# Kernel optimization log

Hardware: AMD Instinct MI355X
Metric: run time of the kernel (lower is better)

## Reference

```python
import jax, jax.numpy as jnp
import numpy as np

B, T, P, F = 32, 12, 128, 128          # batch, timesteps, n_patches, nhid
NODES_PER_PATCH = 64
HORIZON = 12
N_NODES = P * NODES_PER_PATCH          # 8192


def setup_inputs() -> dict:
    key = jax.random.key(0)
    k1, k2, k3, k4 = jax.random.split(key, 4)
    x = jax.random.normal(k1, (B, T, P, F), dtype=jnp.float32)
    # per-patch Linear weights/biases, stacked: W[p] maps (nhid*T) -> (nodes_p*horizon)
    W = jax.random.normal(k2, (P, T * F, NODES_PER_PATCH * HORIZON), dtype=jnp.float32) * 0.02
    b = jax.random.normal(k3, (P, NODES_PER_PATCH * HORIZON), dtype=jnp.float32) * 0.02
    # patch -> global node indices; a permutation (each node in exactly one patch)
    patch_node_map = jax.random.permutation(k4, jnp.arange(N_NODES, dtype=jnp.int64)).reshape(P, NODES_PER_PATCH)
    return {"x": x, "W": W, "b": b, "patch_node_map": patch_node_map}


def reference(x, W, b, patch_node_map):
    # rearrange 'b t p f -> b p (t f)'
    xr = jnp.transpose(x, (0, 2, 1, 3)).reshape(x.shape[0], P, T * F)
    # grouped GEMM: one Linear per patch
    out = jnp.einsum('bpi,pio->bpo', xr, W) + b          # [B, P, nodes*H]
    out = out.reshape(x.shape[0], P * NODES_PER_PATCH, HORIZON)
    # scatter patch-local node predictions to global node positions
    out_all = jnp.zeros((x.shape[0], N_NODES, HORIZON), dtype=x.dtype)
    out_all = out_all.at[:, patch_node_map.reshape(-1), :].set(out)
    return out_all
```

## Files before the change

### kernel.cpp

```cpp
#include <hip/hip_runtime.h>
#include <hip/hip_bf16.h>


constexpr int T      = 12;
constexpr int P      = 128;
constexpr int F      = 128;
constexpr int K      = T * F;
constexpr int N      = 768;
constexpr int NPP    = 64;
constexpr int H      = 12;
constexpr int NNODES = P * NPP;
constexpr int BN     = 384;
constexpr int NSTEP  = 48;
constexpr int TPF    = T * P * F;
constexpr int PF     = P * F;

typedef __attribute__((ext_vector_type(8))) short        bf16x8;
typedef __attribute__((ext_vector_type(4))) float        f32x4;
typedef __attribute__((ext_vector_type(4))) unsigned int u32x4;

__device__ inline unsigned short f2bfu(float f) {
    return __bfloat16_as_ushort(__float2bfloat16(f));
}
__device__ inline unsigned int pk2(float lo, float hi) {
    return (unsigned int)f2bfu(lo) | ((unsigned int)f2bfu(hi) << 16);
}

__global__ __launch_bounds__(384, 1)
void patch_readout_kernel(const float* __restrict__ x,
                          const float* __restrict__ W,
                          const float* __restrict__ bias,
                          const int*   __restrict__ map,
                          float*       __restrict__ out)
{
    __shared__ short Xs[32 * K];
    __shared__ short Ws2[2][4 * BN * 8];
    char* xl  = (char*)&Xs[0];
    char* wlb = (char*)&Ws2[0][0];

    const int bid = blockIdx.x;
    const int lgc = (bid & 7) * 32 + (bid >> 3);
    const int p   = lgc >> 1;
    const int n0  = (lgc & 1) * BN;

    const int tid  = threadIdx.x;
    const int lane = tid & 63;
    const int wv   = tid >> 6;
    const int r    = lane & 15;
    const int c    = lane >> 4;

    const int c2 = tid / 96;
    const int q  = tid - c2 * 96;
    const float* wg = W + (size_t)p * K * N + (size_t)(8 * c2) * N + (n0 + 4 * q);

    f32x4 ws[8];

    auto issueW = [&](int s) {
        #pragma unroll
        for (int j = 0; j < 8; ++j)
            ws[j] = *(const f32x4*)(wg + (size_t)(s * 32 + j) * N);
    };

    auto writeW = [&](int d) {
        char* wl = wlb + d * 24576 + c2 * 6144;
        #pragma unroll
        for (int i = 0; i < 4; ++i) {
            u32x4 wd;
            wd.x = pk2(ws[0][i], ws[1][i]);
            wd.y = pk2(ws[2][i], ws[3][i]);
            wd.z = pk2(ws[4][i], ws[5][i]);
            wd.w = pk2(ws[6][i], ws[7][i]);
            const int col = 4 * q + i;
            *(u32x4*)(wl + ((col * 16) ^ (((col >> 3) & 7) << 4))) = wd;
        }
    };

    auto stageX = [&]() {
        const int row = tid / 12;
        const int sub = tid - row * 12;
        const float* xg = x + (size_t)row * TPF + (size_t)sub * PF + (size_t)p * F;
        char* xw = xl + row * 3072;
        const int sw = (row & 7) << 4;
        #pragma unroll
        for (int ci = 0; ci < 16; ++ci) {
            f32x4 v0 = *(const f32x4*)(xg + ci * 8);
            f32x4 v1 = *(const f32x4*)(xg + ci * 8 + 4);
            bf16x8 xv;
            xv[0] = (short)f2bfu(v0.x); xv[1] = (short)f2bfu(v0.y);
            xv[2] = (short)f2bfu(v0.z); xv[3] = (short)f2bfu(v0.w);
            xv[4] = (short)f2bfu(v1.x); xv[5] = (short)f2bfu(v1.y);
            xv[6] = (short)f2bfu(v1.z); xv[7] = (short)f2bfu(v1.w);
            *(bf16x8*)(xw + ((sub * 256 + ci * 16) ^ sw)) = xv;
        }
    };

    f32x4 acc[2][4] = {};

    auto compute = [&](int s, int d) {
        const char* wl = wlb + d * 24576 + c * 6144;
        bf16x8 af[2];
        #pragma unroll
        for (int mi = 0; mi < 2; ++mi) {
            const int row = mi * 16 + r;
            af[mi] = *(const bf16x8*)(xl + row * 3072 +
                                      ((s * 64 + c * 16) ^ ((row & 7) << 4)));
        }
        #pragma unroll
        for (int ni = 0; ni < 4; ++ni) {
            const int col = wv * 64 + ni * 16 + r;
            bf16x8 bf = *(const bf16x8*)(wl + ((col * 16) ^ (((col >> 3) & 7) << 4)));
            #pragma unroll
            for (int mi = 0; mi < 2; ++mi)
                acc[mi][ni] = __builtin_amdgcn_mfma_f32_16x16x32_bf16(
                    af[mi], bf, acc[mi][ni], 0, 0, 0);
        }
    };

    issueW(0);
    stageX();
    writeW(0);

    for (int s = 0; s < NSTEP; ++s) {
        __syncthreads();
        if (s < NSTEP - 1) issueW(s + 1);
        compute(s, s & 1);
        if (s < NSTEP - 1) writeW((s + 1) & 1);
    }

    #pragma unroll
    for (int ni = 0; ni < 4; ++ni) {
        const int col = n0 + wv * 64 + ni * 16 + r;
        const int nl  = col / H;
        const int h   = col - nl * H;
        const int g   = map[p * NPP + nl];
        const float bv = bias[p * N + col];
        #pragma unroll
        for (int mi = 0; mi < 2; ++mi) {
            #pragma unroll
            for (int i = 0; i < 4; ++i) {
                const int b = mi * 16 + c * 4 + i;
                out[((size_t)b * NNODES + g) * H + h] = acc[mi][ni][i] + bv;
            }
        }
    }
}

extern "C" void kernel_launch(void* const* d_in, const int* in_sizes, int n_in,
                              void* d_out, int out_size, void* d_ws, size_t ws_size,
                              hipStream_t stream) {
    const float* x    = (const float*)d_in[0];
    const float* W    = (const float*)d_in[1];
    const float* bias = (const float*)d_in[2];
    const int*   map  = (const int*)d_in[3];
    float*       out  = (float*)d_out;

    dim3 grid(256);
    dim3 block(384);
    patch_readout_kernel<<<grid, block, 0, stream>>>(x, W, bias, map, out);
}
```

Baseline: 125.2 us.

## Split-K grouped GEMM into two halves with bf16 workspace reduction kernel

```diff
diff --git a/kernel.cpp b/kernel.cpp
--- a/kernel.cpp
+++ b/kernel.cpp
@@ -10,10 +10,12 @@
 constexpr int NPP    = 64;
 constexpr int H      = 12;
 constexpr int NNODES = P * NPP;
-constexpr int BN     = 384;
-constexpr int NSTEP  = 48;
+constexpr int KH2    = 768;
+constexpr int NSTEP2 = KH2 / 32;
 constexpr int TPF    = T * P * F;
 constexpr int PF     = P * F;
+constexpr size_t HALF_ELE = (size_t)P * 32 * N;
+constexpr size_t WS_BYTES = 2 * HALF_ELE * 2;
 
 typedef __attribute__((ext_vector_type(8))) short        bf16x8;
 typedef __attribute__((ext_vector_type(4))) float        f32x4;
@@ -25,23 +27,23 @@
 __device__ inline unsigned int pk2(float lo, float hi) {
     return (unsigned int)f2bfu(lo) | ((unsigned int)f2bfu(hi) << 16);
 }
+__device__ inline f32x4 ntload(const float* p) {
+    return __builtin_nontemporal_load((const f32x4*)p);
+}
 
 __global__ __launch_bounds__(384, 1)
-void patch_readout_kernel(const float* __restrict__ x,
-                          const float* __restrict__ W,
-                          const float* __restrict__ bias,
-                          const int*   __restrict__ map,
-                          float*       __restrict__ out)
+void pr_phase1(const float* __restrict__ x, const float* __restrict__ W,
+               __hip_bfloat16* __restrict__ wsp_out)
 {
-    __shared__ short Xs[32 * K];
-    __shared__ short Ws2[2][4 * BN * 8];
+    __shared__ short Xs[32 * KH2];
+    __shared__ short Ws2[2][4 * N * 8];
     char* xl  = (char*)&Xs[0];
     char* wlb = (char*)&Ws2[0][0];
 
     const int bid = blockIdx.x;
     const int lgc = (bid & 7) * 32 + (bid >> 3);
     const int p   = lgc >> 1;
-    const int n0  = (lgc & 1) * BN;
+    const int kh  = lgc & 1;
 
     const int tid  = threadIdx.x;
     const int lane = tid & 63;
@@ -51,16 +53,158 @@
 
     const int c2 = tid / 96;
     const int q  = tid - c2 * 96;
+    const float* wg = W + (size_t)p * K * N + ((size_t)(kh * KH2 + 8 * c2)) * N + 8 * q;
+
+    f32x4 ws[16];
+
+    auto issueW = [&](int s) {
+        #pragma unroll
+        for (int j = 0; j < 8; ++j) {
+            const float* b = wg + (size_t)(s * 32 + j) * N;
+            ws[2 * j]     = ntload(b);
+            ws[2 * j + 1] = ntload(b + 4);
+        }
+    };
+
+    auto writeW = [&](int d) {
+        char* wl = wlb + d * 49152 + c2 * 12288;
+        #pragma unroll
+        for (int i = 0; i < 8; ++i) {
+            const int hi = i >> 2, lo = i & 3;
+            u32x4 wd;
+            wd.x = pk2(ws[0  + hi][lo], ws[2  + hi][lo]);
+            wd.y = pk2(ws[4  + hi][lo], ws[6  + hi][lo]);
+            wd.z = pk2(ws[8  + hi][lo], ws[10 + hi][lo]);
+            wd.w = pk2(ws[12 + hi][lo], ws[14 + hi][lo]);
+            const int col = 8 * q + i;
+            *(u32x4*)(wl + ((col * 16) ^ ((q & 7) << 4))) = wd;
+        }
+    };
+
+    auto stageX = [&]() {
+        const int row = tid / 12;
+        const int sub = tid - row * 12;
+        const int kg0 = kh * KH2 + sub * 64;
+        const int t   = kg0 >> 7;
+        const int f0  = kg0 & 127;
+        const float* xg = x + (size_t)row * TPF + (size_t)t * PF + (size_t)p * F + f0;
+        char* xw = xl + row * 1536;
+        const int sw = (row & 7) << 4;
+        #pragma unroll
+        for (int ci = 0; ci < 8; ++ci) {
+            f32x4 v0 = *(const f32x4*)(xg + ci * 8);
+            f32x4 v1 = *(const f32x4*)(xg + ci * 8 + 4);
+            bf16x8 xv;
+            xv[0] = (short)f2bfu(v0.x); xv[1] = (short)f2bfu(v0.y);
+            xv[2] = (short)f2bfu(v0.z); xv[3] = (short)f2bfu(v0.w);
+            xv[4] = (short)f2bfu(v1.x); xv[5] = (short)f2bfu(v1.y);
+            xv[6] = (short)f2bfu(v1.z); xv[7] = (short)f2bfu(v1.w);
+            const int ks2 = sub * 128 + ci * 16;
+            *(bf16x8*)(xw + (ks2 ^ sw)) = xv;
+        }
+    };
+
+    f32x4 acc[2][8] = {};
+
+    auto compute = [&](int s, int d) {
+        const char* wl = wlb + d * 49152 + c * 12288;
+        bf16x8 af[2];
+        #pragma unroll
+        for (int mi = 0; mi < 2; ++mi) {
+            const int row = mi * 16 + r;
+            af[mi] = *(const bf16x8*)(xl + row * 1536 +
+                                      ((s * 64 + c * 16) ^ ((row & 7) << 4)));
+        }
+        #pragma unroll
+        for (int ni = 0; ni < 8; ++ni) {
+            const int col = wv * 128 + ni * 16 + r;
+            bf16x8 bf = *(const bf16x8*)(wl + ((col * 16) ^ (((col >> 3) & 7) << 4)));
+            #pragma unroll
+            for (int mi = 0; mi < 2; ++mi)
+                acc[mi][ni] = __builtin_amdgcn_mfma_f32_16x16x32_bf16(
+                    af[mi], bf, acc[mi][ni], 0, 0, 0);
+        }
+    };
+
+    issueW(0);
+    stageX();
+    writeW(0);
+    __syncthreads();
+    issueW(1);
+
+    for (int kt = 0; kt < NSTEP2; ++kt) {
+        compute(kt, kt & 1);
+        if (kt < NSTEP2 - 1) {
+            writeW((kt + 1) & 1);
+            __syncthreads();
+            if (kt < NSTEP2 - 2) issueW(kt + 2);
+        }
+    }
+
+    __hip_bfloat16* wsp = wsp_out + ((size_t)(kh * P + p) * 32) * N;
+    #pragma unroll
+    for (int ni = 0; ni < 8; ++ni) {
+        const int col = wv * 128 + ni * 16 + r;
+        #pragma unroll
+        for (int mi = 0; mi < 2; ++mi) {
+            #pragma unroll
+            for (int i = 0; i < 4; ++i) {
+                const int b = mi * 16 + c * 4 + i;
+                wsp[(size_t)b * N + col] = __float2bfloat16(acc[mi][ni][i]);
+            }
+        }
+    }
+}
+
+__global__ __launch_bounds__(256)
+void pr_phase2(const __hip_bfloat16* __restrict__ wsp, const float* __restrict__ bias,
+               const int* __restrict__ map, float* __restrict__ out)
+{
+    const size_t idx = (size_t)blockIdx.x * 256 + threadIdx.x;
+    if (idx >= HALF_ELE) return;
+    const int col = (int)(idx % N);
+    const size_t rem = idx / N;
+    const int b = (int)(rem & 31);
+    const int p = (int)(rem >> 5);
+    const float v = __bfloat162float(wsp[idx]) + __bfloat162float(wsp[idx + HALF_ELE])
+                  + bias[p * N + col];
+    const int nl = col / H;
+    const int h  = col - nl * H;
+    const int g  = map[p * NPP + nl];
+    out[((size_t)b * NNODES + g) * H + h] = v;
+}
+
+__global__ __launch_bounds__(384, 1)
+void pr_fallback(const float* __restrict__ x, const float* __restrict__ W,
+                 const float* __restrict__ bias, const int* __restrict__ map,
+                 float* __restrict__ out)
+{
+    __shared__ short Xs[32 * K];
+    __shared__ short Ws2[2][4 * 384 * 8];
+    char* xl  = (char*)&Xs[0];
+    char* wlb = (char*)&Ws2[0][0];
+
+    const int bid = blockIdx.x;
+    const int lgc = (bid & 7) * 32 + (bid >> 3);
+    const int p   = lgc >> 1;
+    const int n0  = (lgc & 1) * 384;
+
+    const int tid  = threadIdx.x;
+    const int lane = tid & 63;
+    const int wv   = tid >> 6;
+    const int r    = lane & 15;
+    const int c    = lane >> 4;
+
+    const int c2 = tid / 96;
+    const int q  = tid - c2 * 96;
     const float* wg = W + (size_t)p * K * N + (size_t)(8 * c2) * N + (n0 + 4 * q);
 
     f32x4 ws[8];
-
     auto issueW = [&](int s) {
         #pragma unroll
         for (int j = 0; j < 8; ++j)
             ws[j] = *(const f32x4*)(wg + (size_t)(s * 32 + j) * N);
     };
-
     auto writeW = [&](int d) {
         char* wl = wlb + d * 24576 + c2 * 6144;
         #pragma unroll
@@ -74,7 +218,6 @@
             *(u32x4*)(wl + ((col * 16) ^ (((col >> 3) & 7) << 4))) = wd;
         }
     };
-
     auto stageX = [&]() {
         const int row = tid / 12;
         const int sub = tid - row * 12;
@@ -95,7 +238,6 @@
     };
 
     f32x4 acc[2][4] = {};
-
     auto compute = [&](int s, int d) {
         const char* wl = wlb + d * 24576 + c * 6144;
         bf16x8 af[2];
@@ -116,15 +258,16 @@
         }
     };
 
-    issueW(0);
-    stageX();
-    writeW(0);
-
-    for (int s = 0; s < NSTEP; ++s) {
-        __syncthreads();
-        if (s < NSTEP - 1) issueW(s + 1);
-        compute(s, s & 1);
-        if (s < NSTEP - 1) writeW((s + 1) & 1);
+    issueW(0); stageX(); writeW(0);
+    __syncthreads();
+    issueW(1);
+    for (int kt = 0; kt < 48; ++kt) {
+        compute(kt, kt & 1);
+        if (kt < 47) {
+            writeW((kt + 1) & 1);
+            __syncthreads();
+            if (kt < 46) issueW(kt + 2);
+        }
     }
 
     #pragma unroll
@@ -154,7 +297,12 @@
     const int*   map  = (const int*)d_in[3];
     float*       out  = (float*)d_out;
 
-    dim3 grid(256);
-    dim3 block(384);
-    patch_readout_kernel<<<grid, block, 0, stream>>>(x, W, bias, map, out);
-}
+    if (ws_size >= WS_BYTES) {
+        pr_phase1<<<dim3(256), dim3(384), 0, stream>>>(x, W, (__hip_bfloat16*)d_ws);
+        const int g2 = (int)((HALF_ELE + 255) / 256);
+        pr_phase2<<<dim3(g2), dim3(256), 0, stream>>>((const __hip_bfloat16*)d_ws,
+                                                      bias, map, out);
+    } else {
+        pr_fallback<<<dim3(256), dim3(384), 0, stream>>>(x, W, bias, map, out);
+    }
+}
```

Result: slower. 137.7 us (+9.9%).

## Stream W directly into LDS via global_load_lds and convert at compute time

Applied to the files above, without the earlier changes.

```diff
diff --git a/kernel.cpp b/kernel.cpp
--- a/kernel.cpp
+++ b/kernel.cpp
@@ -15,15 +15,14 @@
 constexpr int TPF    = T * P * F;
 constexpr int PF     = P * F;
 
-typedef __attribute__((ext_vector_type(8))) short        bf16x8;
-typedef __attribute__((ext_vector_type(4))) float        f32x4;
-typedef __attribute__((ext_vector_type(4))) unsigned int u32x4;
+typedef __attribute__((ext_vector_type(8))) short  bf16x8;
+typedef __attribute__((ext_vector_type(4))) float  f32x4;
+
+typedef __attribute__((address_space(1))) const void  gvoid_t;
+typedef __attribute__((address_space(3))) void        lvoid_t;
 
 __device__ inline unsigned short f2bfu(float f) {
     return __bfloat16_as_ushort(__float2bfloat16(f));
-}
-__device__ inline unsigned int pk2(float lo, float hi) {
-    return (unsigned int)f2bfu(lo) | ((unsigned int)f2bfu(hi) << 16);
 }
 
 __global__ __launch_bounds__(384, 1)
@@ -33,10 +32,9 @@
                           const int*   __restrict__ map,
                           float*       __restrict__ out)
 {
-    __shared__ short Xs[32 * K];
-    __shared__ short Ws2[2][4 * BN * 8];
-    char* xl  = (char*)&Xs[0];
-    char* wlb = (char*)&Ws2[0][0];
+    __shared__ short Xs[32 * 768];
+    __shared__ float Wl[2][32 * BN];
+    char* xl = (char*)&Xs[0];
 
     const int bid = blockIdx.x;
     const int lgc = (bid & 7) * 32 + (bid >> 3);
@@ -49,40 +47,36 @@
     const int r    = lane & 15;
     const int c    = lane >> 4;
 
-    const int c2 = tid / 96;
-    const int q  = tid - c2 * 96;
-    const float* wg = W + (size_t)p * K * N + (size_t)(8 * c2) * N + (n0 + 4 * q);
+    const char* WpB = (const char*)(W + (size_t)p * K * N + n0);
+    const char* wsrc[8];
+    #pragma unroll
+    for (int i = 0; i < 8; ++i) {
+        const int flat = wv * 8192 + i * 1024 + lane * 16;
+        const int k    = flat / 1536;
+        const int rb   = flat - k * 1536;
+        wsrc[i] = WpB + (size_t)k * 3072 + rb;
+    }
 
-    f32x4 ws[8];
-
-    auto issueW = [&](int s) {
+    auto issueW = [&](int kt, int d) {
+        char* ldsb = (char*)&Wl[d][0] + wv * 8192;
+        const size_t go = (size_t)kt * 98304;
         #pragma unroll
-        for (int j = 0; j < 8; ++j)
-            ws[j] = *(const f32x4*)(wg + (size_t)(s * 32 + j) * N);
+        for (int i = 0; i < 8; ++i)
+            __builtin_amdgcn_global_load_lds((gvoid_t*)(wsrc[i] + go),
+                                             (lvoid_t*)(ldsb + i * 1024), 16, 0, 0);
     };
 
-    auto writeW = [&](int d) {
-        char* wl = wlb + d * 24576 + c2 * 6144;
-        #pragma unroll
-        for (int i = 0; i < 4; ++i) {
-            u32x4 wd;
-            wd.x = pk2(ws[0][i], ws[1][i]);
-            wd.y = pk2(ws[2][i], ws[3][i]);
-            wd.z = pk2(ws[4][i], ws[5][i]);
-            wd.w = pk2(ws[6][i], ws[7][i]);
-            const int col = 4 * q + i;
-            *(u32x4*)(wl + ((col * 16) ^ (((col >> 3) & 7) << 4))) = wd;
-        }
-    };
-
-    auto stageX = [&]() {
+    auto stageX = [&](int half) {
         const int row = tid / 12;
         const int sub = tid - row * 12;
-        const float* xg = x + (size_t)row * TPF + (size_t)sub * PF + (size_t)p * F;
-        char* xw = xl + row * 3072;
+        const int kg0 = half * 768 + sub * 64;
+        const int t   = kg0 >> 7;
+        const int f0  = kg0 & 127;
+        const float* xg = x + (size_t)row * TPF + (size_t)t * PF + (size_t)p * F + f0;
+        char* xw = xl + row * 1536;
         const int sw = (row & 7) << 4;
         #pragma unroll
-        for (int ci = 0; ci < 16; ++ci) {
+        for (int ci = 0; ci < 8; ++ci) {
             f32x4 v0 = *(const f32x4*)(xg + ci * 8);
             f32x4 v1 = *(const f32x4*)(xg + ci * 8 + 4);
             bf16x8 xv;
@@ -90,41 +84,51 @@
             xv[2] = (short)f2bfu(v0.z); xv[3] = (short)f2bfu(v0.w);
             xv[4] = (short)f2bfu(v1.x); xv[5] = (short)f2bfu(v1.y);
             xv[6] = (short)f2bfu(v1.z); xv[7] = (short)f2bfu(v1.w);
-            *(bf16x8*)(xw + ((sub * 256 + ci * 16) ^ sw)) = xv;
+            *(bf16x8*)(xw + ((sub * 128 + ci * 16) ^ sw)) = xv;
         }
     };
 
     f32x4 acc[2][4] = {};
 
-    auto compute = [&](int s, int d) {
-        const char* wl = wlb + d * 24576 + c * 6144;
+    auto compute = [&](int sl, int d) {
         bf16x8 af[2];
         #pragma unroll
         for (int mi = 0; mi < 2; ++mi) {
             const int row = mi * 16 + r;
-            af[mi] = *(const bf16x8*)(xl + row * 3072 +
-                                      ((s * 64 + c * 16) ^ ((row & 7) << 4)));
+            af[mi] = *(const bf16x8*)(xl + row * 1536 +
+                                      ((sl * 64 + c * 16) ^ ((row & 7) << 4)));
         }
+        const float* wt = &Wl[d][0];
         #pragma unroll
         for (int ni = 0; ni < 4; ++ni) {
             const int col = wv * 64 + ni * 16 + r;
-            bf16x8 bf = *(const bf16x8*)(wl + ((col * 16) ^ (((col >> 3) & 7) << 4)));
+            const float* wc = wt + (8 * c) * BN + col;
+            bf16x8 bfv;
+            #pragma unroll
+            for (int j = 0; j < 8; ++j)
+                bfv[j] = (short)f2bfu(wc[j * BN]);
             #pragma unroll
             for (int mi = 0; mi < 2; ++mi)
                 acc[mi][ni] = __builtin_amdgcn_mfma_f32_16x16x32_bf16(
-                    af[mi], bf, acc[mi][ni], 0, 0, 0);
+                    af[mi], bfv, acc[mi][ni], 0, 0, 0);
         }
     };
 
-    issueW(0);
-    stageX();
-    writeW(0);
+    issueW(0, 0);
+    stageX(0);
+    __syncthreads();
+    issueW(1, 1);
 
-    for (int s = 0; s < NSTEP; ++s) {
-        __syncthreads();
-        if (s < NSTEP - 1) issueW(s + 1);
-        compute(s, s & 1);
-        if (s < NSTEP - 1) writeW((s + 1) & 1);
+    for (int kt = 0; kt < NSTEP; ++kt) {
+        if (kt == 24) {
+            stageX(1);
+            __syncthreads();
+        }
+        compute(kt >= 24 ? kt - 24 : kt, kt & 1);
+        if (kt < NSTEP - 1) {
+            __syncthreads();
+            if (kt < NSTEP - 2) issueW(kt + 2, kt & 1);
+        }
     }
 
     #pragma unroll
```

New measurement: 122.3 us. -2.4%, faster.
